# Kernel tuning notes

Measured on AMD Instinct MI355X. Metric: run time of the kernel, lower is better.

Reference implementation:

```python
import jax, jax.numpy as jnp
import numpy as np

Q_DIM, KV_DIM, H = 64, 64, 4


def setup_inputs() -> dict:
    key = jax.random.key(0)
    ks = jax.random.split(key, 8)
    b, t = 8, 128
    q_x = jax.random.normal(ks[0], (b, t, Q_DIM), dtype=jnp.float32)
    kv_x = jax.random.normal(ks[1], (b, t, t - 1, KV_DIM), dtype=jnp.float32)
    # nn.Linear weights: (out_features, in_features), applied as x @ W.T
    Wk = jax.random.normal(ks[2], (KV_DIM * H, KV_DIM), dtype=jnp.float32) * 0.05
    Wq = jax.random.normal(ks[3], (KV_DIM * H, Q_DIM), dtype=jnp.float32) * 0.05
    Wv = jax.random.normal(ks[4], (KV_DIM * H, KV_DIM), dtype=jnp.float32) * 0.05
    bias = jax.random.uniform(ks[5], (KV_DIM,), minval=-0.1, maxval=0.1, dtype=jnp.float32)
    Ws = jax.random.normal(ks[6], (1, KV_DIM), dtype=jnp.float32) * 0.05
    bs = jax.random.normal(ks[7], (1,), dtype=jnp.float32) * 0.05
    return {"q_x": q_x, "kv_x": kv_x, "Wk": Wk, "Wq": Wq, "Wv": Wv,
            "bias": bias, "Ws": Ws, "bs": bs}


def reference(q_x, kv_x, Wk, Wq, Wv, bias, Ws, bs):
    b, t, tm1, k = kv_x.shape  # tm1 == t-1
    h = H
    # keys: (b, t, t-1, h, k)
    keys = (kv_x @ Wk.T).reshape(b, t, tm1, h, k)
    # queries: (b, t, 1, h, k)
    queries = (q_x @ Wq.T).reshape(b, t, 1, h, k)
    # additive tanh score projected to scalar per (b,t,n,h)
    act = jnp.tanh(keys + queries + bias)
    score = jnp.einsum('btnhk,k->btnh', act, Ws[0]) + bs[0]
    # softmax over the t-1 key axis (dim=2)
    w = jax.nn.softmax(score, axis=2)  # (b, t, t-1, h)
    values = (kv_x @ Wv.T).reshape(b, t, tm1, h, k)
    # weighted sum over t-1
    x = jnp.einsum('btnh,btnhk->bthk', w, values)
    return x.reshape(b, t, h * k)
```

## Files before the change

### kernel.cpp

```cpp
#include <hip/hip_runtime.h>
#include <math.h>

#define B 8
#define T 128
#define NKEY 127
#define NPAD 128
#define KDIM 64
#define NH 4
#define CH 256

typedef short short8 __attribute__((ext_vector_type(8)));
typedef float floatx4 __attribute__((ext_vector_type(4)));

__device__ __forceinline__ float fast_tanh(float x) {
    float e = __expf(2.f * x);
    float r = __builtin_amdgcn_rcpf(e + 1.f);
    return fmaf(-2.f, r, 1.f);
}

__device__ __forceinline__ void split8(const float4& a, const float4& b,
                                       short8& hi, short8& lo) {
    float x[8] = {a.x, a.y, a.z, a.w, b.x, b.y, b.z, b.w};
    #pragma unroll
    for (int i = 0; i < 8; ++i) {
        unsigned u = __float_as_uint(x[i]);
        hi[i] = (short)(u >> 16);
        float l = x[i] - __uint_as_float(u & 0xFFFF0000u);
        lo[i] = (short)(__float_as_uint(l) >> 16);
    }
}

__global__ __launch_bounds__(256, 2)
void attn_kernel(const float* __restrict__ q_x,
                 const float* __restrict__ kv_x,
                 const float* __restrict__ Wk,
                 const float* __restrict__ Wq,
                 const float* __restrict__ Wv,
                 const float* __restrict__ bias,
                 const float* __restrict__ Ws,
                 const float* __restrict__ bs,
                 float* __restrict__ out)
{
    __shared__ float kv_lds[NPAD][KDIM];
    __shared__ float q_lds[KDIM];
    __shared__ float qb_lds[CH];
    __shared__ float p_lds[NH][NPAD];
    __shared__ float wkv_lds[NH][KDIM];
    __shared__ __align__(16) short bh_lds[16][64][8];
    __shared__ __align__(16) short bl_lds[16][64][8];

    const int bt   = blockIdx.x;
    const int tid  = threadIdx.x;
    const int h    = tid >> 6;
    const int lane = tid & 63;
    const int col  = lane & 15;
    const int quad = lane >> 4;

    if (tid < KDIM) q_lds[tid] = q_x[(size_t)bt * KDIM + tid];
    {
        const float4* src = (const float4*)(kv_x + (size_t)bt * NKEY * KDIM);
        float4* dst = (float4*)(&kv_lds[0][0]);
        for (int i = tid; i < NPAD * KDIM / 4; i += 256) {
            float4 v = make_float4(0.f, 0.f, 0.f, 0.f);
            if (i < NKEY * KDIM / 4) v = src[i];
            dst[i] = v;
        }
    }
    __syncthreads();

    {
        const float4* Wq4 = (const float4*)(Wq + (size_t)tid * KDIM);
        float4 qa = {0.f, 0.f, 0.f, 0.f};
        #pragma unroll
        for (int i = 0; i < 16; ++i) {
            float4 w = Wq4[i];
            float4 q4 = ((const float4*)q_lds)[i];
            qa.x = fmaf(q4.x, w.x, qa.x);
            qa.y = fmaf(q4.y, w.y, qa.y);
            qa.z = fmaf(q4.z, w.z, qa.z);
            qa.w = fmaf(q4.w, w.w, qa.w);
        }
        qb_lds[tid] = (qa.x + qa.y) + (qa.z + qa.w) + bias[tid & 63];
    }

    {
        const int chunk = tid >> 4;
        const int ks    = chunk & 1;
        const int nt    = chunk >> 1;
        const int fl0   = (tid & 15) * 4;
        #pragma unroll
        for (int w = 0; w < 4; ++w) {
            int fl = fl0 + w;
            int n  = nt * 16 + (fl & 15);
            int k0 = ks * 32 + (fl >> 4) * 8;
            float4 a = *(const float4*)&kv_lds[n][k0];
            float4 b = *(const float4*)&kv_lds[n][k0 + 4];
            short8 hi, lo;
            split8(a, b, hi, lo);
            *(short8*)&bh_lds[chunk][fl][0] = hi;
            *(short8*)&bl_lds[chunk][fl][0] = lo;
        }
    }
    __syncthreads();

    short8 ahi[4][2], alo[4][2];
    #pragma unroll
    for (int jt = 0; jt < 4; ++jt)
        #pragma unroll
        for (int ks = 0; ks < 2; ++ks) {
            const float* wrow = Wk + (size_t)(h * 64 + jt * 16 + col) * KDIM
                                   + ks * 32 + quad * 8;
            float4 a = *(const float4*)wrow;
            float4 b = *(const float4*)(wrow + 4);
            split8(a, b, ahi[jt][ks], alo[jt][ks]);
        }

    float qbv[4][4], wsv[4][4];
    #pragma unroll
    for (int jt = 0; jt < 4; ++jt)
        #pragma unroll
        for (int r = 0; r < 4; ++r) {
            int j = jt * 16 + quad * 4 + r;
            qbv[jt][r] = qb_lds[h * 64 + j];
            wsv[jt][r] = Ws[j];
        }

    for (int nt = 0; nt < 8; ++nt) {
        short8 bhi0 = *(const short8*)&bh_lds[nt * 2 + 0][lane][0];
        short8 blo0 = *(const short8*)&bl_lds[nt * 2 + 0][lane][0];
        short8 bhi1 = *(const short8*)&bh_lds[nt * 2 + 1][lane][0];
        short8 blo1 = *(const short8*)&bl_lds[nt * 2 + 1][lane][0];

        floatx4 acc[4];
        #pragma unroll
        for (int jt = 0; jt < 4; ++jt) {
            floatx4 c = {0.f, 0.f, 0.f, 0.f};
            c = __builtin_amdgcn_mfma_f32_16x16x32_bf16(ahi[jt][0], bhi0, c, 0, 0, 0);
            c = __builtin_amdgcn_mfma_f32_16x16x32_bf16(ahi[jt][1], bhi1, c, 0, 0, 0);
            c = __builtin_amdgcn_mfma_f32_16x16x32_bf16(ahi[jt][0], blo0, c, 0, 0, 0);
            c = __builtin_amdgcn_mfma_f32_16x16x32_bf16(ahi[jt][1], blo1, c, 0, 0, 0);
            c = __builtin_amdgcn_mfma_f32_16x16x32_bf16(alo[jt][0], bhi0, c, 0, 0, 0);
            c = __builtin_amdgcn_mfma_f32_16x16x32_bf16(alo[jt][1], bhi1, c, 0, 0, 0);
            acc[jt] = c;
        }

        float partial = 0.f;
        #pragma unroll
        for (int jt = 0; jt < 4; ++jt)
            #pragma unroll
            for (int r = 0; r < 4; ++r)
                partial = fmaf(fast_tanh(acc[jt][r] + qbv[jt][r]), wsv[jt][r], partial);
        partial += __shfl_xor(partial, 16, 64);
        partial += __shfl_xor(partial, 32, 64);
        if (lane < 16) p_lds[h][nt * 16 + lane] = partial;
    }

    float invl;
    {
        float s_a = p_lds[h][lane];
        float s_b = p_lds[h][64 + lane];
        if (lane == 63) s_b = -1e30f;
        float mx = fmaxf(s_a, s_b);
        #pragma unroll
        for (int off = 32; off > 0; off >>= 1)
            mx = fmaxf(mx, __shfl_xor(mx, off, 64));
        float pa = __expf(s_a - mx);
        float pb = __expf(s_b - mx);
        float ls = pa + pb;
        #pragma unroll
        for (int off = 32; off > 0; off >>= 1)
            ls += __shfl_xor(ls, off, 64);
        invl = 1.f / ls;
        p_lds[h][lane]      = pa;
        p_lds[h][64 + lane] = pb;
    }

    {
        float w0 = 0.f, w1 = 0.f, w2 = 0.f, w3 = 0.f;
        #pragma unroll 4
        for (int n4 = 0; n4 < NPAD; n4 += 4) {
            float4 p4 = *(const float4*)&p_lds[h][n4];
            w0 = fmaf(p4.x, kv_lds[n4 + 0][lane], w0);
            w1 = fmaf(p4.y, kv_lds[n4 + 1][lane], w1);
            w2 = fmaf(p4.z, kv_lds[n4 + 2][lane], w2);
            w3 = fmaf(p4.w, kv_lds[n4 + 3][lane], w3);
        }
        wkv_lds[h][lane] = ((w0 + w1) + (w2 + w3)) * invl;
    }

    {
        const float4* Wv4 = (const float4*)(Wv + (size_t)tid * KDIM);
        const float4* wv_row = (const float4*)wkv_lds[h];
        float4 oa = {0.f, 0.f, 0.f, 0.f};
        #pragma unroll
        for (int i = 0; i < 16; ++i) {
            float4 w = Wv4[i];
            float4 c = wv_row[i];
            oa.x = fmaf(c.x, w.x, oa.x);
            oa.y = fmaf(c.y, w.y, oa.y);
            oa.z = fmaf(c.z, w.z, oa.z);
            oa.w = fmaf(c.w, w.w, oa.w);
        }
        out[(size_t)bt * CH + tid] = (oa.x + oa.y) + (oa.z + oa.w);
    }
}

extern "C" void kernel_launch(void* const* d_in, const int* in_sizes, int n_in,
                              void* d_out, int out_size, void* d_ws, size_t ws_size,
                              hipStream_t stream) {
    const float* q_x  = (const float*)d_in[0];
    const float* kv_x = (const float*)d_in[1];
    const float* Wk   = (const float*)d_in[2];
    const float* Wq   = (const float*)d_in[3];
    const float* Wv   = (const float*)d_in[4];
    const float* bias = (const float*)d_in[5];
    const float* Ws   = (const float*)d_in[6];
    const float* bs   = (const float*)d_in[7];
    float* out = (float*)d_out;

    attn_kernel<<<dim3(B * T), dim3(256), 0, stream>>>(
        q_x, kv_x, Wk, Wq, Wv, bias, Ws, bs, out);
}
```

Measured before the change: 122.6 us.

## Drop kv staging buffer, split kv directly from global, raise occupancy

Removes the fp32 kv_x LDS staging tile (32KB) and the q_x LDS copy. The kernel now loads kv rows straight from global memory into the bf16 hi/lo split buffers and re-reads kv_x from global (expected to hit in cache) for the weighted sum. Launch bounds move to 4 blocks per CU and one barrier is removed, which frees LDS and aims for more concurrent blocks. The cost is repeated global/L2 reads of kv_x in the weighted-sum loop and tighter register limits.

```diff
diff --git a/kernel.cpp b/kernel.cpp
--- a/kernel.cpp
+++ b/kernel.cpp
@@ -30,7 +30,7 @@
     }
 }
 
-__global__ __launch_bounds__(256, 2)
+__global__ __launch_bounds__(256, 4)
 void attn_kernel(const float* __restrict__ q_x,
                  const float* __restrict__ kv_x,
                  const float* __restrict__ Wk,
@@ -41,13 +41,11 @@
                  const float* __restrict__ bs,
                  float* __restrict__ out)
 {
-    __shared__ float kv_lds[NPAD][KDIM];
-    __shared__ float q_lds[KDIM];
+    __shared__ __align__(16) short bh_lds[16][64][8];
+    __shared__ __align__(16) short bl_lds[16][64][8];
     __shared__ float qb_lds[CH];
     __shared__ float p_lds[NH][NPAD];
     __shared__ float wkv_lds[NH][KDIM];
-    __shared__ __align__(16) short bh_lds[16][64][8];
-    __shared__ __align__(16) short bl_lds[16][64][8];
 
     const int bt   = blockIdx.x;
     const int tid  = threadIdx.x;
@@ -56,25 +54,35 @@
     const int col  = lane & 15;
     const int quad = lane >> 4;
 
-    if (tid < KDIM) q_lds[tid] = q_x[(size_t)bt * KDIM + tid];
-    {
-        const float4* src = (const float4*)(kv_x + (size_t)bt * NKEY * KDIM);
-        float4* dst = (float4*)(&kv_lds[0][0]);
-        for (int i = tid; i < NPAD * KDIM / 4; i += 256) {
-            float4 v = make_float4(0.f, 0.f, 0.f, 0.f);
-            if (i < NKEY * KDIM / 4) v = src[i];
-            dst[i] = v;
-        }
-    }
-    __syncthreads();
+    const float* __restrict__ kvg = kv_x + (size_t)bt * NKEY * KDIM;
+
+    #pragma unroll
+    for (int w = 0; w < 4; ++w) {
+        const int chunk = w * 4 + h;
+        const int nt = chunk >> 1, ks = chunk & 1;
+        const int n  = nt * 16 + (lane & 15);
+        const int k0 = ks * 32 + (lane >> 4) * 8;
+        float4 a = make_float4(0.f, 0.f, 0.f, 0.f);
+        float4 b = make_float4(0.f, 0.f, 0.f, 0.f);
+        if (n < NKEY) {
+            const float* p = kvg + (size_t)n * KDIM + k0;
+            a = *(const float4*)p;
+            b = *(const float4*)(p + 4);
+        }
+        short8 hi, lo;
+        split8(a, b, hi, lo);
+        *(short8*)&bh_lds[chunk][lane][0] = hi;
+        *(short8*)&bl_lds[chunk][lane][0] = lo;
+    }
 
     {
         const float4* Wq4 = (const float4*)(Wq + (size_t)tid * KDIM);
+        const float4* q4g = (const float4*)(q_x + (size_t)bt * KDIM);
         float4 qa = {0.f, 0.f, 0.f, 0.f};
         #pragma unroll
         for (int i = 0; i < 16; ++i) {
             float4 w = Wq4[i];
-            float4 q4 = ((const float4*)q_lds)[i];
+            float4 q4 = q4g[i];
             qa.x = fmaf(q4.x, w.x, qa.x);
             qa.y = fmaf(q4.y, w.y, qa.y);
             qa.z = fmaf(q4.z, w.z, qa.z);
@@ -82,26 +90,6 @@
         }
         qb_lds[tid] = (qa.x + qa.y) + (qa.z + qa.w) + bias[tid & 63];
     }
-
-    {
-        const int chunk = tid >> 4;
-        const int ks    = chunk & 1;
-        const int nt    = chunk >> 1;
-        const int fl0   = (tid & 15) * 4;
-        #pragma unroll
-        for (int w = 0; w < 4; ++w) {
-            int fl = fl0 + w;
-            int n  = nt * 16 + (fl & 15);
-            int k0 = ks * 32 + (fl >> 4) * 8;
-            float4 a = *(const float4*)&kv_lds[n][k0];
-            float4 b = *(const float4*)&kv_lds[n][k0 + 4];
-            short8 hi, lo;
-            split8(a, b, hi, lo);
-            *(short8*)&bh_lds[chunk][fl][0] = hi;
-            *(short8*)&bl_lds[chunk][fl][0] = lo;
-        }
-    }
-    __syncthreads();
 
     short8 ahi[4][2], alo[4][2];
     #pragma unroll
@@ -114,6 +102,8 @@
             float4 b = *(const float4*)(wrow + 4);
             split8(a, b, ahi[jt][ks], alo[jt][ks]);
         }
+
+    __syncthreads();
 
     float qbv[4][4], wsv[4][4];
     #pragma unroll
@@ -177,13 +167,14 @@
 
     {
         float w0 = 0.f, w1 = 0.f, w2 = 0.f, w3 = 0.f;
-        #pragma unroll 4
+        #pragma unroll 8
         for (int n4 = 0; n4 < NPAD; n4 += 4) {
             float4 p4 = *(const float4*)&p_lds[h][n4];
-            w0 = fmaf(p4.x, kv_lds[n4 + 0][lane], w0);
-            w1 = fmaf(p4.y, kv_lds[n4 + 1][lane], w1);
-            w2 = fmaf(p4.z, kv_lds[n4 + 2][lane], w2);
-            w3 = fmaf(p4.w, kv_lds[n4 + 3][lane], w3);
+            const int n3 = (n4 + 3 < NKEY) ? (n4 + 3) : 0;
+            w0 = fmaf(p4.x, kvg[(size_t)(n4 + 0) * KDIM + lane], w0);
+            w1 = fmaf(p4.y, kvg[(size_t)(n4 + 1) * KDIM + lane], w1);
+            w2 = fmaf(p4.z, kvg[(size_t)(n4 + 2) * KDIM + lane], w2);
+            w3 = fmaf(p4.w, kvg[(size_t)n3 * KDIM + lane], w3);
         }
         wkv_lds[h][lane] = ((w0 + w1) + (w2 + w3)) * invl;
     }
```

Measured after the change: 127.0 us. 3.5% more time.
